# Performance work log

Measured on AMD Instinct MI355X. Metric: run time of the kernel, lower is better.

Reference implementation:

```python
import jax, jax.numpy as jnp
import numpy as np

EPS = 1e-5


def _whiten(X, T):
    # X: (B, C, H, W); group whitening with g=1, d=C, m=B*H*W
    B, C, H, W = X.shape
    g, d = 1, C
    x = jnp.transpose(X, (1, 0, 2, 3)).reshape(g, d, -1)  # (g, d, m)
    m = x.shape[-1]
    mean = jnp.mean(x, axis=-1, keepdims=True)
    xc = x - mean
    I = jnp.broadcast_to(jnp.eye(d, dtype=X.dtype)[None], (g, d, d))
    Sigma = EPS * I + jnp.einsum('gim,gjm->gij', xc, xc) / m
    rTr = 1.0 / jnp.trace(Sigma, axis1=1, axis2=2)[:, None, None]  # 1/tr(Sigma)
    Sigma_N = Sigma * rTr
    P = I
    for _ in range(T):  # Newton-Schulz: P <- 1.5*P - 0.5*P^3 @ Sigma_N
        P = 1.5 * P - 0.5 * (P @ P @ P @ Sigma_N)
    wm = P * jnp.sqrt(rTr)  # inverse sqrt of Sigma
    xn = jnp.einsum('gij,gjm->gim', wm, xc)  # (g, d, m)
    return jnp.transpose(xn.reshape(C, B, H, W), (1, 0, 2, 3))


def reference(X, rot, T):
    # mode = -1: whiten then rotate with running_rot, affine=False
    B, C, H, W = X.shape
    g = rot.shape[0]
    d = C // g
    Xn = _whiten(X, T)                       # (B, C, H, W)
    Xh = Xn.reshape(B, g, d, H, W)
    Xr = jnp.einsum('bgchw,gdc->bgdhw', Xh, rot)
    return Xr.reshape(B, C, H, W)


def setup_inputs() -> dict:
    key = jax.random.key(0)
    k1, k2 = jax.random.split(key)
    X = jax.random.normal(k1, (32, 512, 56, 56), dtype=jnp.float32)
    # running_rot buffer; use a random orthogonal matrix for realism
    A = jax.random.normal(k2, (512, 512), dtype=jnp.float32)
    Q, _ = jnp.linalg.qr(A)
    rot = Q[None]  # (1, 512, 512)
    return {"X": X, "rot": rot, "T": 10}
```

## Files before the change

### kernel.cpp

```cpp
#include <hip/hip_runtime.h>
#include <hip/hip_bf16.h>

typedef __bf16 v8bf __attribute__((ext_vector_type(8)));
typedef float  v4f  __attribute__((ext_vector_type(4)));
typedef unsigned short u16;
typedef unsigned int   u32;

#define GAS __attribute__((address_space(1)))
#define LAS __attribute__((address_space(3)))

constexpr int C_ = 512;
constexpr int S_ = 3136;
constexpr int B_ = 32;
constexpr int M_ = B_ * S_;
constexpr float INV_M = 1.0f / (float)M_;

__device__ __forceinline__ void async16(const u16* g, u16* l) {
  __builtin_amdgcn_global_load_lds((const GAS u32*)g, (LAS u32*)l, 16, 0, 0);
}

__device__ __forceinline__ u16 f2bf(float f) {
  u32 u = __builtin_bit_cast(u32, f);
  u += 0x7fffu + ((u >> 16) & 1u);
  return (u16)(u >> 16);
}

__global__ __launch_bounds__(256) void prep_kernel(const float* __restrict__ X,
        u16* __restrict__ xbf, u16* __restrict__ xbfT, float* __restrict__ chsum) {
  __shared__ u16 Ts[64 * 65];
  const int tid = threadIdx.x;
  const int s0 = blockIdx.x * 64;
  const int c0 = blockIdx.y * 64;
  const int b  = blockIdx.z;

  const int i  = tid >> 2;
  const int jc = (tid & 3) * 16;
  const float* xp = X + (b * C_ + c0 + i) * S_ + s0 + jc;
  u16* op = xbf + (c0 + i) * M_ + b * S_ + s0 + jc;
  float ssum = 0.f;
  #pragma unroll
  for (int u = 0; u < 4; ++u) {
    float4 xv = *(const float4*)(xp + u * 4);
    ssum += xv.x + xv.y + xv.z + xv.w;
    u16 e0 = f2bf(xv.x), e1 = f2bf(xv.y), e2 = f2bf(xv.z), e3 = f2bf(xv.w);
    *(ushort4*)(op + u * 4) = make_ushort4(e0, e1, e2, e3);
    const int lb = i * 65 + jc + u * 4;
    Ts[lb + 0] = e0; Ts[lb + 1] = e1; Ts[lb + 2] = e2; Ts[lb + 3] = e3;
  }
  ssum += __shfl_down(ssum, 2, 4);
  ssum += __shfl_down(ssum, 1, 4);
  if ((tid & 3) == 0) atomicAdd(&chsum[c0 + i], ssum);
  __syncthreads();

  const int lane = tid & 63, wv = tid >> 6;
  #pragma unroll
  for (int p = 0; p < 2; ++p) {
    const int j  = p * 32 + wv * 8 + (lane >> 3);
    const int cc = (lane & 7) * 8;
    u16 tmp[8];
    #pragma unroll
    for (int e = 0; e < 8; ++e) tmp[e] = Ts[(cc + e) * 65 + j];
    u16* tp = xbfT + (b * S_ + s0 + j) * C_ + c0 + cc;
    *(ushort4*)(tp + 0) = make_ushort4(tmp[0], tmp[1], tmp[2], tmp[3]);
    *(ushort4*)(tp + 4) = make_ushort4(tmp[4], tmp[5], tmp[6], tmp[7]);
  }
}

__global__ __launch_bounds__(256, 2) void sigma_gemm(const u16* __restrict__ xbf,
                                                     float* __restrict__ part) {
  __shared__ u16 As[128 * 64];
  __shared__ u16 Bs[128 * 64];
  const int tid = threadIdx.x;
  const int tj = blockIdx.x, ti = blockIdx.y, z = blockIdx.z;
  const int kbase = z * S_;
  const int srow = tid >> 3;
  const int scol = (tid & 7) * 8;
  const int lane = tid & 63, wv = tid >> 6;
  const int wm = (wv & 1) * 64, wn = (wv >> 1) * 64;
  const int lr = lane & 15, lq = lane >> 4;
  const u16* gA = xbf + (ti * 128) * M_ + kbase + scol;
  const u16* gB = xbf + (tj * 128) * M_ + kbase + scol;
  v4f acc[4][4] = {};
  for (int it = 0; it < 49; ++it) {
    const int k0 = it * 64;
    #pragma unroll
    for (int q = 0; q < 4; ++q) {
      const int r = q * 32 + srow;
      async16(gA + r * M_ + k0, &As[r * 64 + scol]);
      async16(gB + r * M_ + k0, &Bs[r * 64 + scol]);
    }
    __syncthreads();
    #pragma unroll
    for (int kk = 0; kk < 2; ++kk) {
      v8bf a[4], b[4];
      #pragma unroll
      for (int x = 0; x < 4; ++x) a[x] = *(const v8bf*)&As[(wm + x*16 + lr)*64 + kk*32 + lq*8];
      #pragma unroll
      for (int x = 0; x < 4; ++x) b[x] = *(const v8bf*)&Bs[(wn + x*16 + lr)*64 + kk*32 + lq*8];
      #pragma unroll
      for (int mi = 0; mi < 4; ++mi)
        #pragma unroll
        for (int ni = 0; ni < 4; ++ni)
          acc[mi][ni] = __builtin_amdgcn_mfma_f32_16x16x32_bf16(a[mi], b[ni], acc[mi][ni], 0, 0, 0);
    }
    __syncthreads();
  }
  float* op = part + z * (C_ * C_);
  #pragma unroll
  for (int mi = 0; mi < 4; ++mi) {
    const int gi = ti * 128 + wm + mi * 16 + lq * 4;
    #pragma unroll
    for (int ni = 0; ni < 4; ++ni) {
      const int gj = tj * 128 + wn + ni * 16 + lr;
      #pragma unroll
      for (int r = 0; r < 4; ++r)
        op[(gi + r) * C_ + gj] = acc[mi][ni][r];
    }
  }
}

__global__ __launch_bounds__(256) void reduce_sigma(const float* __restrict__ part,
        const float* __restrict__ chsum, float* __restrict__ Sigma,
        float* __restrict__ trace) {
  const int idx = blockIdx.x * 256 + threadIdx.x;
  const int i = idx >> 9, j = idx & 511;
  float s = 0.f;
  #pragma unroll 8
  for (int z = 0; z < 32; ++z) s += part[z * (C_ * C_) + idx];
  float val = s * INV_M - (chsum[i] * INV_M) * (chsum[j] * INV_M);
  if (i == j) val += 1e-5f;
  Sigma[idx] = val;
  if (i == j) atomicAdd(trace, val);
}

__global__ __launch_bounds__(256) void init_ns(const float* __restrict__ Sigma,
        const float* __restrict__ trace, float* __restrict__ SN, float* __restrict__ P) {
  const int idx = blockIdx.x * 256 + threadIdx.x;
  const float rtr = 1.0f / trace[0];
  SN[idx] = Sigma[idx] * rtr;
  P[idx] = ((idx >> 9) == (idx & 511)) ? 1.0f : 0.f;
}

__global__ __launch_bounds__(256) void mm512_kernel(
    const float* __restrict__ A, const float* __restrict__ Bz0, float* __restrict__ Cz0,
    const float* __restrict__ Bz1, float* __restrict__ Cz1,
    float* __restrict__ P, const float* __restrict__ trace, u16* __restrict__ Cbf,
    const int* __restrict__ Tptr, int iter, int mode) {
  if (Tptr && iter >= Tptr[0]) return;
  const float* Bp = (blockIdx.z == 0) ? Bz0 : Bz1;
  float*       Cp = (blockIdx.z == 0) ? Cz0 : Cz1;
  __shared__ float As[32 * 36];
  __shared__ float Bs[32 * 36];
  const int tid = threadIdx.x;
  const int ro = tid >> 3;
  const int co = (tid & 7) * 4;
  const int ti = blockIdx.y * 32, tj = blockIdx.x * 32;
  float a0 = 0.f, a1 = 0.f, a2 = 0.f, a3 = 0.f;
  for (int k0 = 0; k0 < 512; k0 += 32) {
    float4 av = *(const float4*)(A  + (ti + ro) * 512 + k0 + co);
    float4 bv = *(const float4*)(Bp + (k0 + ro) * 512 + tj + co);
    *(float4*)&As[ro * 36 + co] = av;
    *(float4*)&Bs[ro * 36 + co] = bv;
    __syncthreads();
    #pragma unroll
    for (int k = 0; k < 32; ++k) {
      const float a = As[ro * 36 + k];
      const float4 b = *(const float4*)&Bs[k * 36 + co];
      a0 = fmaf(a, b.x, a0); a1 = fmaf(a, b.y, a1);
      a2 = fmaf(a, b.z, a2); a3 = fmaf(a, b.w, a3);
    }
    __syncthreads();
  }
  const int oidx = (ti + ro) * 512 + tj + co;
  if (mode == 0) {
    Cp[oidx + 0] = a0; Cp[oidx + 1] = a1; Cp[oidx + 2] = a2; Cp[oidx + 3] = a3;
  } else if (mode == 1) {
    float4 pv = *(const float4*)(P + oidx);
    pv.x = 1.5f * pv.x - 0.5f * a0;
    pv.y = 1.5f * pv.y - 0.5f * a1;
    pv.z = 1.5f * pv.z - 0.5f * a2;
    pv.w = 1.5f * pv.w - 0.5f * a3;
    *(float4*)(P + oidx) = pv;
  } else {
    const float sc = sqrtf(1.0f / trace[0]);
    a0 *= sc; a1 *= sc; a2 *= sc; a3 *= sc;
    Cp[oidx + 0] = a0; Cp[oidx + 1] = a1; Cp[oidx + 2] = a2; Cp[oidx + 3] = a3;
    *(ushort4*)(Cbf + oidx) = make_ushort4(f2bf(a0), f2bf(a1), f2bf(a2), f2bf(a3));
  }
}

__global__ __launch_bounds__(256) void calc_v(const float* __restrict__ M2f,
        const float* __restrict__ chsum, float* __restrict__ v) {
  const int d = blockIdx.x * 256 + threadIdx.x;
  float s = 0.f;
  for (int c = 0; c < 512; ++c) s += M2f[d * 512 + c] * (chsum[c] * INV_M);
  v[d] = s;
}

__global__ __launch_bounds__(256, 2) void out_gemm(const u16* __restrict__ Abf,
        const u16* __restrict__ Bt, const float* __restrict__ v, float* __restrict__ out) {
  __shared__ u16 As[128 * 64];
  __shared__ u16 Bs[128 * 64];
  const int tid = threadIdx.x;
  const int tn = blockIdx.x, td = blockIdx.y;
  const int srow = tid >> 3, scol = (tid & 7) * 8;
  const int lane = tid & 63, wv = tid >> 6;
  const int wm = (wv & 1) * 64, wn = (wv >> 1) * 64;
  const int lr = lane & 15, lq = lane >> 4;
  const u16* gA = Abf + (td * 128) * 512 + scol;
  const u16* gB = Bt + (tn * 128) * 512 + scol;
  v4f acc[4][4] = {};
  for (int it = 0; it < 8; ++it) {
    const int k0 = it * 64;
    #pragma unroll
    for (int q = 0; q < 4; ++q) {
      const int r = q * 32 + srow;
      async16(gA + r * 512 + k0, &As[r * 64 + scol]);
      async16(gB + r * 512 + k0, &Bs[r * 64 + scol]);
    }
    __syncthreads();
    #pragma unroll
    for (int kk = 0; kk < 2; ++kk) {
      v8bf a[4], b[4];
      #pragma unroll
      for (int x = 0; x < 4; ++x) a[x] = *(const v8bf*)&As[(wm + x*16 + lr)*64 + kk*32 + lq*8];
      #pragma unroll
      for (int x = 0; x < 4; ++x) b[x] = *(const v8bf*)&Bs[(wn + x*16 + lr)*64 + kk*32 + lq*8];
      #pragma unroll
      for (int mi = 0; mi < 4; ++mi)
        #pragma unroll
        for (int ni = 0; ni < 4; ++ni)
          acc[mi][ni] = __builtin_amdgcn_mfma_f32_16x16x32_bf16(a[mi], b[ni], acc[mi][ni], 0, 0, 0);
    }
    __syncthreads();
  }
  #pragma unroll
  for (int mi = 0; mi < 4; ++mi) {
    const int d0 = td * 128 + wm + mi * 16 + lq * 4;
    const float vd0 = v[d0 + 0], vd1 = v[d0 + 1], vd2 = v[d0 + 2], vd3 = v[d0 + 3];
    #pragma unroll
    for (int ni = 0; ni < 4; ++ni) {
      const unsigned mcol = tn * 128 + wn + ni * 16 + lr;
      const unsigned bb = mcol / 3136u;
      const unsigned ss = mcol - bb * 3136u;
      const int obase = (int)(bb * 512u) * 3136 + (int)ss;
      out[obase + (d0 + 0) * 3136] = acc[mi][ni][0] - vd0;
      out[obase + (d0 + 1) * 3136] = acc[mi][ni][1] - vd1;
      out[obase + (d0 + 2) * 3136] = acc[mi][ni][2] - vd2;
      out[obase + (d0 + 3) * 3136] = acc[mi][ni][3] - vd3;
    }
  }
}

extern "C" void kernel_launch(void* const* d_in, const int* in_sizes, int n_in,
                              void* d_out, int out_size, void* d_ws, size_t ws_size,
                              hipStream_t stream) {
  const float* X   = (const float*)d_in[0];
  const float* rot = (const float*)d_in[1];
  const int*   T   = (const int*)d_in[2];
  float* out = (float*)d_out;

  char* ws = (char*)d_ws;
  size_t off = 0;
  auto alloc = [&](size_t bytes) -> char* {
    char* p = ws + off;
    off += (bytes + 255) & ~(size_t)255;
    return p;
  };
  u16*   xbf   = (u16*)alloc((size_t)C_ * M_ * 2);
  u16*   xbfT  = (u16*)alloc((size_t)M_ * C_ * 2);
  float* part  = (float*)alloc((size_t)32 * C_ * C_ * 4);
  float* Sigma = (float*)alloc((size_t)C_ * C_ * 4);
  float* SN    = (float*)alloc((size_t)C_ * C_ * 4);
  float* P     = (float*)alloc((size_t)C_ * C_ * 4);
  float* T1    = (float*)alloc((size_t)C_ * C_ * 4);
  float* T2    = (float*)alloc((size_t)C_ * C_ * 4);
  float* M2f   = (float*)alloc((size_t)C_ * C_ * 4);
  u16*   M2bf  = (u16*)alloc((size_t)C_ * C_ * 2);
  float* chsum = (float*)alloc(2048);
  float* trace = (float*)alloc(256);
  float* v     = (float*)alloc(2048);
  (void)ws_size; (void)in_sizes; (void)n_in; (void)out_size;

  hipMemsetAsync(chsum, 0, 2048 + 256, stream);

  prep_kernel<<<dim3(49, 8, 32), 256, 0, stream>>>(X, xbf, xbfT, chsum);
  sigma_gemm<<<dim3(4, 4, 32), 256, 0, stream>>>(xbf, part);
  reduce_sigma<<<dim3(1024), 256, 0, stream>>>(part, chsum, Sigma, trace);
  init_ns<<<dim3(1024), 256, 0, stream>>>(Sigma, trace, SN, P);

  for (int iter = 0; iter < 10; ++iter) {
    mm512_kernel<<<dim3(16, 16, 2), 256, 0, stream>>>(P, P, T1, SN, T2, P, trace, M2bf, T, iter, 0);
    mm512_kernel<<<dim3(16, 16, 1), 256, 0, stream>>>(T1, T2, T1, T2, T1, P, trace, M2bf, T, iter, 1);
  }
  mm512_kernel<<<dim3(16, 16, 1), 256, 0, stream>>>(rot, P, M2f, P, M2f, P, trace, M2bf, nullptr, 0, 2);
  calc_v<<<dim3(2), 256, 0, stream>>>(M2f, chsum, v);
  out_gemm<<<dim3(784, 4), 256, 0, stream>>>(M2bf, xbfT, v, out);
}
```

Baseline: 906.8 us.

## Fuse Newton-Schulz iterations into one cooperative kernel using split-bf16 MFMA

```diff
diff --git a/kernel.cpp b/kernel.cpp
--- a/kernel.cpp
+++ b/kernel.cpp
@@ -1,5 +1,8 @@
 #include <hip/hip_runtime.h>
 #include <hip/hip_bf16.h>
+#include <hip/hip_cooperative_groups.h>
+
+namespace cg = cooperative_groups;
 
 typedef __bf16 v8bf __attribute__((ext_vector_type(8)));
 typedef float  v4f  __attribute__((ext_vector_type(4)));
@@ -23,6 +26,9 @@
   u32 u = __builtin_bit_cast(u32, f);
   u += 0x7fffu + ((u >> 16) & 1u);
   return (u16)(u >> 16);
+}
+__device__ __forceinline__ float bf2f(u16 h) {
+  return __builtin_bit_cast(float, (u32)h << 16);
 }
 
 __global__ __launch_bounds__(256) void prep_kernel(const float* __restrict__ X,
@@ -119,82 +125,166 @@
   }
 }
 
-__global__ __launch_bounds__(256) void reduce_sigma(const float* __restrict__ part,
-        const float* __restrict__ chsum, float* __restrict__ Sigma,
-        float* __restrict__ trace) {
-  const int idx = blockIdx.x * 256 + threadIdx.x;
-  const int i = idx >> 9, j = idx & 511;
-  float s = 0.f;
-  #pragma unroll 8
-  for (int z = 0; z < 32; ++z) s += part[z * (C_ * C_) + idx];
-  float val = s * INV_M - (chsum[i] * INV_M) * (chsum[j] * INV_M);
-  if (i == j) val += 1e-5f;
-  Sigma[idx] = val;
-  if (i == j) atomicAdd(trace, val);
-}
-
-__global__ __launch_bounds__(256) void init_ns(const float* __restrict__ Sigma,
-        const float* __restrict__ trace, float* __restrict__ SN, float* __restrict__ P) {
-  const int idx = blockIdx.x * 256 + threadIdx.x;
-  const float rtr = 1.0f / trace[0];
-  SN[idx] = Sigma[idx] * rtr;
-  P[idx] = ((idx >> 9) == (idx & 511)) ? 1.0f : 0.f;
-}
-
-__global__ __launch_bounds__(256) void mm512_kernel(
-    const float* __restrict__ A, const float* __restrict__ Bz0, float* __restrict__ Cz0,
-    const float* __restrict__ Bz1, float* __restrict__ Cz1,
-    float* __restrict__ P, const float* __restrict__ trace, u16* __restrict__ Cbf,
-    const int* __restrict__ Tptr, int iter, int mode) {
-  if (Tptr && iter >= Tptr[0]) return;
-  const float* Bp = (blockIdx.z == 0) ? Bz0 : Bz1;
-  float*       Cp = (blockIdx.z == 0) ? Cz0 : Cz1;
-  __shared__ float As[32 * 36];
-  __shared__ float Bs[32 * 36];
+struct CoopArgs {
+  const float* part; const float* chsum; const float* rotf; const int* Tptr;
+  float* trace; float* Sigma;
+  u16 *SNh, *SNl, *Ph, *Pl, *T1h, *T1l, *T2h, *T2l;
+  float* Pf; u16 *roth, *rotl; float* M2f; u16* M2bf; float* v;
+};
+
+__global__ __launch_bounds__(256, 2) void ns_coop(CoopArgs A) {
+  cg::grid_group grid = cg::this_grid();
+  __shared__ float comb[2][256];
   const int tid = threadIdx.x;
-  const int ro = tid >> 3;
-  const int co = (tid & 7) * 4;
-  const int ti = blockIdx.y * 32, tj = blockIdx.x * 32;
-  float a0 = 0.f, a1 = 0.f, a2 = 0.f, a3 = 0.f;
-  for (int k0 = 0; k0 < 512; k0 += 32) {
-    float4 av = *(const float4*)(A  + (ti + ro) * 512 + k0 + co);
-    float4 bv = *(const float4*)(Bp + (k0 + ro) * 512 + tj + co);
-    *(float4*)&As[ro * 36 + co] = av;
-    *(float4*)&Bs[ro * 36 + co] = bv;
+  const int b = blockIdx.x;
+  const int lane = tid & 63, wv = tid >> 6;
+  const int gw = b * 4 + wv;
+  const int lr = lane & 15, lq = lane >> 4;
+
+  {
+    const float mb = A.chsum[b] * INV_M;
+    for (int c = tid; c < 512; c += 256) {
+      float s = 0.f;
+      #pragma unroll 8
+      for (int z = 0; z < 32; ++z) s += A.part[z * 262144 + b * 512 + c];
+      float val = s * INV_M - mb * (A.chsum[c] * INV_M);
+      if (c == b) { val += 1e-5f; atomicAdd(A.trace, val); }
+      A.Sigma[b * 512 + c] = val;
+    }
+  }
+  __threadfence();
+  grid.sync();
+  const float rtr = 1.0f / A.trace[0];
+
+  for (int c = tid; c < 512; c += 256) {
+    const int idx = b * 512 + c;
+    float sn = A.Sigma[idx] * rtr;
+    u16 h = f2bf(sn); A.SNh[idx] = h; A.SNl[idx] = f2bf(sn - bf2f(h));
+    float pv = (b == c) ? 1.0f : 0.f;
+    A.Pf[idx] = pv; A.Ph[idx] = f2bf(pv); A.Pl[idx] = 0;
+    float rv = A.rotf[idx];
+    u16 rh = f2bf(rv); A.roth[idx] = rh; A.rotl[idx] = f2bf(rv - bf2f(rh));
+  }
+  __threadfence();
+  grid.sync();
+
+  const int T = A.Tptr[0];
+  for (int it = 0; it < T; ++it) {
+    {
+      const int sel = gw >> 10, t = gw & 1023;
+      const int tr = t >> 5, tc = t & 31;
+      const u16* pa  = A.Ph + (tr * 16 + lr) * 512 + lq * 8;
+      const u16* pal = A.Pl + (tr * 16 + lr) * 512 + lq * 8;
+      const u16* pb  = (sel ? A.SNh : A.Ph) + (tc * 16 + lr) * 512 + lq * 8;
+      const u16* pbl = (sel ? A.SNl : A.Pl) + (tc * 16 + lr) * 512 + lq * 8;
+      v4f acc = {0.f, 0.f, 0.f, 0.f};
+      #pragma unroll 4
+      for (int k = 0; k < 512; k += 32) {
+        v8bf ah = *(const v8bf*)(pa + k);
+        v8bf al = *(const v8bf*)(pal + k);
+        v8bf bh = *(const v8bf*)(pb + k);
+        v8bf bl = *(const v8bf*)(pbl + k);
+        acc = __builtin_amdgcn_mfma_f32_16x16x32_bf16(ah, bh, acc, 0, 0, 0);
+        acc = __builtin_amdgcn_mfma_f32_16x16x32_bf16(ah, bl, acc, 0, 0, 0);
+        acc = __builtin_amdgcn_mfma_f32_16x16x32_bf16(al, bh, acc, 0, 0, 0);
+      }
+      u16* Dh = sel ? A.T2h : A.T1h;
+      u16* Dl = sel ? A.T2l : A.T1l;
+      #pragma unroll
+      for (int r = 0; r < 4; ++r) {
+        const int idx = (tr * 16 + lq * 4 + r) * 512 + tc * 16 + lr;
+        float x = acc[r];
+        u16 h = f2bf(x); Dh[idx] = h; Dl[idx] = f2bf(x - bf2f(h));
+      }
+    }
+    __threadfence();
+    grid.sync();
+    {
+      const int t = gw >> 1, h = gw & 1;
+      const int tr = t >> 5, tc = t & 31;
+      const int kb = h * 256;
+      const u16* pa  = A.T1h + (tr * 16 + lr) * 512 + kb + lq * 8;
+      const u16* pal = A.T1l + (tr * 16 + lr) * 512 + kb + lq * 8;
+      const u16* pb  = A.T2h + (tc * 16 + lr) * 512 + kb + lq * 8;
+      const u16* pbl = A.T2l + (tc * 16 + lr) * 512 + kb + lq * 8;
+      v4f acc = {0.f, 0.f, 0.f, 0.f};
+      #pragma unroll 4
+      for (int k = 0; k < 256; k += 32) {
+        v8bf ah = *(const v8bf*)(pa + k);
+        v8bf al = *(const v8bf*)(pal + k);
+        v8bf bh = *(const v8bf*)(pb + k);
+        v8bf bl = *(const v8bf*)(pbl + k);
+        acc = __builtin_amdgcn_mfma_f32_16x16x32_bf16(ah, bh, acc, 0, 0, 0);
+        acc = __builtin_amdgcn_mfma_f32_16x16x32_bf16(ah, bl, acc, 0, 0, 0);
+        acc = __builtin_amdgcn_mfma_f32_16x16x32_bf16(al, bh, acc, 0, 0, 0);
+      }
+      const int pair = wv >> 1;
+      if (h == 1) *(v4f*)&comb[pair][lane * 4] = acc;
+      __syncthreads();
+      if (h == 0) {
+        v4f o = *(const v4f*)&comb[pair][lane * 4];
+        #pragma unroll
+        for (int r = 0; r < 4; ++r) {
+          const int idx = (tr * 16 + lq * 4 + r) * 512 + tc * 16 + lr;
+          float nv = 1.5f * A.Pf[idx] - 0.5f * (acc[r] + o[r]);
+          A.Pf[idx] = nv;
+          u16 hh = f2bf(nv); A.Ph[idx] = hh; A.Pl[idx] = f2bf(nv - bf2f(hh));
+        }
+      }
+    }
+    __threadfence();
+    grid.sync();
+  }
+
+  {
+    const int t = gw >> 1, h = gw & 1;
+    const int tr = t >> 5, tc = t & 31;
+    const int kb = h * 256;
+    const u16* pa  = A.roth + (tr * 16 + lr) * 512 + kb + lq * 8;
+    const u16* pal = A.rotl + (tr * 16 + lr) * 512 + kb + lq * 8;
+    const u16* pb  = A.Ph + (tc * 16 + lr) * 512 + kb + lq * 8;
+    const u16* pbl = A.Pl + (tc * 16 + lr) * 512 + kb + lq * 8;
+    v4f acc = {0.f, 0.f, 0.f, 0.f};
+    #pragma unroll 4
+    for (int k = 0; k < 256; k += 32) {
+      v8bf ah = *(const v8bf*)(pa + k);
+      v8bf al = *(const v8bf*)(pal + k);
+      v8bf bh = *(const v8bf*)(pb + k);
+      v8bf bl = *(const v8bf*)(pbl + k);
+      acc = __builtin_amdgcn_mfma_f32_16x16x32_bf16(ah, bh, acc, 0, 0, 0);
+      acc = __builtin_amdgcn_mfma_f32_16x16x32_bf16(ah, bl, acc, 0, 0, 0);
+      acc = __builtin_amdgcn_mfma_f32_16x16x32_bf16(al, bh, acc, 0, 0, 0);
+    }
+    const int pair = wv >> 1;
+    if (h == 1) *(v4f*)&comb[pair][lane * 4] = acc;
     __syncthreads();
-    #pragma unroll
-    for (int k = 0; k < 32; ++k) {
-      const float a = As[ro * 36 + k];
-      const float4 b = *(const float4*)&Bs[k * 36 + co];
-      a0 = fmaf(a, b.x, a0); a1 = fmaf(a, b.y, a1);
-      a2 = fmaf(a, b.z, a2); a3 = fmaf(a, b.w, a3);
-    }
-    __syncthreads();
-  }
-  const int oidx = (ti + ro) * 512 + tj + co;
-  if (mode == 0) {
-    Cp[oidx + 0] = a0; Cp[oidx + 1] = a1; Cp[oidx + 2] = a2; Cp[oidx + 3] = a3;
-  } else if (mode == 1) {
-    float4 pv = *(const float4*)(P + oidx);
-    pv.x = 1.5f * pv.x - 0.5f * a0;
-    pv.y = 1.5f * pv.y - 0.5f * a1;
-    pv.z = 1.5f * pv.z - 0.5f * a2;
-    pv.w = 1.5f * pv.w - 0.5f * a3;
-    *(float4*)(P + oidx) = pv;
-  } else {
-    const float sc = sqrtf(1.0f / trace[0]);
-    a0 *= sc; a1 *= sc; a2 *= sc; a3 *= sc;
-    Cp[oidx + 0] = a0; Cp[oidx + 1] = a1; Cp[oidx + 2] = a2; Cp[oidx + 3] = a3;
-    *(ushort4*)(Cbf + oidx) = make_ushort4(f2bf(a0), f2bf(a1), f2bf(a2), f2bf(a3));
-  }
-}
-
-__global__ __launch_bounds__(256) void calc_v(const float* __restrict__ M2f,
-        const float* __restrict__ chsum, float* __restrict__ v) {
-  const int d = blockIdx.x * 256 + threadIdx.x;
-  float s = 0.f;
-  for (int c = 0; c < 512; ++c) s += M2f[d * 512 + c] * (chsum[c] * INV_M);
-  v[d] = s;
+    if (h == 0) {
+      v4f o = *(const v4f*)&comb[pair][lane * 4];
+      const float sc = sqrtf(rtr);
+      #pragma unroll
+      for (int r = 0; r < 4; ++r) {
+        const int idx = (tr * 16 + lq * 4 + r) * 512 + tc * 16 + lr;
+        float val = (acc[r] + o[r]) * sc;
+        A.M2f[idx] = val;
+        A.M2bf[idx] = f2bf(val);
+      }
+    }
+  }
+  __threadfence();
+  grid.sync();
+
+  if (gw < 512) {
+    const int d = gw;
+    float s = 0.f;
+    #pragma unroll
+    for (int j = 0; j < 8; ++j) {
+      const int c = lane + j * 64;
+      s += A.M2f[d * 512 + c] * (A.chsum[c] * INV_M);
+    }
+    #pragma unroll
+    for (int off = 32; off; off >>= 1) s += __shfl_down(s, off);
+    if (lane == 0) A.v[d] = s;
+  }
 }
 
 __global__ __launch_bounds__(256, 2) void out_gemm(const u16* __restrict__ Abf,
@@ -271,29 +361,41 @@
   u16*   xbfT  = (u16*)alloc((size_t)M_ * C_ * 2);
   float* part  = (float*)alloc((size_t)32 * C_ * C_ * 4);
   float* Sigma = (float*)alloc((size_t)C_ * C_ * 4);
-  float* SN    = (float*)alloc((size_t)C_ * C_ * 4);
-  float* P     = (float*)alloc((size_t)C_ * C_ * 4);
-  float* T1    = (float*)alloc((size_t)C_ * C_ * 4);
-  float* T2    = (float*)alloc((size_t)C_ * C_ * 4);
-  float* M2f   = (float*)alloc((size_t)C_ * C_ * 4);
-  u16*   M2bf  = (u16*)alloc((size_t)C_ * C_ * 2);
   float* chsum = (float*)alloc(2048);
   float* trace = (float*)alloc(256);
   float* v     = (float*)alloc(2048);
   (void)ws_size; (void)in_sizes; (void)n_in; (void)out_size;
 
+  constexpr size_t HMB = (size_t)C_ * C_ * 2;
+  char* pr = (char*)part;
+  u16*   SNh  = (u16*)(pr + 0 * HMB);
+  u16*   SNl  = (u16*)(pr + 1 * HMB);
+  u16*   Ph   = (u16*)(pr + 2 * HMB);
+  u16*   Pl   = (u16*)(pr + 3 * HMB);
+  u16*   T1h  = (u16*)(pr + 4 * HMB);
+  u16*   T1l  = (u16*)(pr + 5 * HMB);
+  u16*   T2h  = (u16*)(pr + 6 * HMB);
+  u16*   T2l  = (u16*)(pr + 7 * HMB);
+  float* Pf   = (float*)(pr + 8 * HMB);
+  u16*   roth = (u16*)(pr + 10 * HMB);
+  u16*   rotl = (u16*)(pr + 11 * HMB);
+  float* M2f  = (float*)(pr + 12 * HMB);
+  u16*   M2bf = (u16*)(pr + 14 * HMB);
+
   hipMemsetAsync(chsum, 0, 2048 + 256, stream);
 
   prep_kernel<<<dim3(49, 8, 32), 256, 0, stream>>>(X, xbf, xbfT, chsum);
   sigma_gemm<<<dim3(4, 4, 32), 256, 0, stream>>>(xbf, part);
-  reduce_sigma<<<dim3(1024), 256, 0, stream>>>(part, chsum, Sigma, trace);
-  init_ns<<<dim3(1024), 256, 0, stream>>>(Sigma, trace, SN, P);
-
-  for (int iter = 0; iter < 10; ++iter) {
-    mm512_kernel<<<dim3(16, 16, 2), 256, 0, stream>>>(P, P, T1, SN, T2, P, trace, M2bf, T, iter, 0);
-    mm512_kernel<<<dim3(16, 16, 1), 256, 0, stream>>>(T1, T2, T1, T2, T1, P, trace, M2bf, T, iter, 1);
-  }
-  mm512_kernel<<<dim3(16, 16, 1), 256, 0, stream>>>(rot, P, M2f, P, M2f, P, trace, M2bf, nullptr, 0, 2);
-  calc_v<<<dim3(2), 256, 0, stream>>>(M2f, chsum, v);
+
+  CoopArgs ca;
+  ca.part = part; ca.chsum = chsum; ca.rotf = rot; ca.Tptr = T;
+  ca.trace = trace; ca.Sigma = Sigma;
+  ca.SNh = SNh; ca.SNl = SNl; ca.Ph = Ph; ca.Pl = Pl;
+  ca.T1h = T1h; ca.T1l = T1l; ca.T2h = T2h; ca.T2l = T2l;
+  ca.Pf = Pf; ca.roth = roth; ca.rotl = rotl; ca.M2f = M2f; ca.M2bf = M2bf;
+  ca.v = v;
+  void* params[] = { &ca };
+  hipLaunchCooperativeKernel((void*)ns_coop, dim3(512), dim3(256), params, 0, stream);
+
   out_gemm<<<dim3(784, 4), 256, 0, stream>>>(M2bf, xbfT, v, out);
 }
```

After: 3.331 ms. +267.3%, slower.
